# Kernel optimization log

Measured on AMD Instinct MI355X. Metric: run time of the kernel, lower is better.

The kernel has to match this reference:

```python
import jax, jax.numpy as jnp
import numpy as np

B, G, N, D = 8, 16, 256, 768
E, S, SEQ = 1536, 128, 512
EPS = 1e-05


def rope_gn(x):
    # x: [b, g, n, h, s]; positions run over flattened (g, n), matching rope(x, dim=[1,2])
    g, n, half = x.shape[1], x.shape[2], x.shape[-1] // 2
    position = jnp.arange(g * n, dtype=jnp.float32).reshape(g, n)[:, :, None]  # [g,n,1]
    inv_freq = 10000.0 ** (jnp.arange(half, dtype=jnp.float32) / half)
    sinusoid = position[..., None] * inv_freq  # [g,n,1,half]
    sin, cos = jnp.sin(sinusoid), jnp.cos(sinusoid)
    x1, x2 = jnp.split(x, 2, axis=-1)
    return jnp.concatenate([x1 * cos - x2 * sin, x2 * cos + x1 * sin], axis=-1)


def rel_pos_bias(w, seq_len):
    # Toeplitz construction (seq_len <= 512 branch). w: [2*seq_len-1] -> [1, seq_len, seq_len]
    t = jnp.pad(w, (0, seq_len))                  # [3*seq_len-1]
    t = jnp.tile(t, seq_len)[:-seq_len]           # [seq_len*(3*seq_len-2)]
    t = t.reshape(seq_len, 3 * seq_len - 2)
    r = seq_len - 1                                # (2*seq_len-1)//2
    return t[:, r:-r][None]                        # [1, seq_len, seq_len]


def setup_inputs():
    key = jax.random.key(0)
    ks = jax.random.split(key, 8)
    inputs = jax.random.normal(ks[0], (B, G, N, D), dtype=jnp.float32)
    seg = jax.random.randint(ks[1], (B, G * N), 0, 4)
    segment_ids = jnp.sort(seg, axis=-1).reshape(B, G, N)
    params = {
        'ln_w': jnp.ones((D,), jnp.float32),
        'ln_b': jnp.zeros((D,), jnp.float32),
        'W1': jax.random.normal(ks[2], (D, 2 * E + S), jnp.float32) * 0.02,
        'b1': jnp.zeros((2 * E + S,), jnp.float32),
        'gamma': jax.random.uniform(ks[3], (4, S), jnp.float32),
        'beta': jax.random.uniform(ks[4], (4, S), jnp.float32),
        'W2': jax.random.normal(ks[5], (E, D), jnp.float32) * 0.02,
        'b2': jnp.zeros((D,), jnp.float32),
        'w_rel': jax.random.uniform(ks[6], (2 * SEQ - 1,), jnp.float32),
    }
    return dict(inputs=inputs, segment_ids=segment_ids, **params)


def reference(inputs, segment_ids, ln_w, ln_b, W1, b1, gamma, beta, W2, b2, w_rel):
    b, g, n, d = inputs.shape
    shortcut = inputs
    # LayerNorm
    mu = inputs.mean(-1, keepdims=True)
    var = ((inputs - mu) ** 2).mean(-1, keepdims=True)
    x = (inputs - mu) * jax.lax.rsqrt(var + EPS) * ln_w + ln_b
    # dense1 + silu, split into u, v, z
    uv = jax.nn.silu(x @ W1 + b1)
    u, v, z = uv[..., :E], uv[..., E:2 * E], uv[..., 2 * E:]
    # per-head affine gating + rope
    z = z[..., None, :] * gamma + beta            # [b,g,n,4,s]
    z = rope_gn(z)
    quad_q, quad_k, lin_q, lin_k = (z[..., i, :] for i in range(4))
    # non-causal global linear attention
    kv = jnp.einsum('bgcs,bgce->bse', lin_k, v)
    lin_v = jnp.einsum('bgcs,bse->bgce', lin_q, kv)
    lin_kv = jnp.einsum('bgnk,bgne->bgke', lin_k, lin_v) / n
    # segment mask over chunks
    mn = segment_ids.min(-1)
    mx = segment_ids.max(-1)
    mask = ((mn[:, :, None] <= mx[:, None, :]) & (mx[:, :, None] >= mn[:, None, :])).astype(inputs.dtype)
    mask = mask / mask.sum(-1, keepdims=True)
    lin_kv = jnp.einsum('bhke,bgh->bgke', lin_kv, mask)
    linear = jnp.einsum('bgnk,bgke->bgne', lin_q, lin_kv)
    # quadratic relu^2 attention with relative position bias
    qk = jnp.einsum('bgnk,bgmk->bgnm', quad_q, quad_k)
    bias = rel_pos_bias(w_rel, SEQ)[:, :n, :n]    # [1,n,n] broadcasts to [b,g,n,n]
    kernel = jnp.square(jax.nn.relu(qk / n + bias))
    quadratic = jnp.einsum('bgnm,bgme->bgne', kernel, v)
    out = (u * (quadratic + linear)) @ W2 + b2 + shortcut
    return out
```

## Files before the change

### kernel.cpp

```cpp
#include <hip/hip_runtime.h>
#include <math.h>

typedef __bf16 bf16;
typedef __bf16 bf16x8 __attribute__((ext_vector_type(8)));
typedef __bf16 bf16x4 __attribute__((ext_vector_type(4)));
typedef float  f32x4  __attribute__((ext_vector_type(4)));

#define D_   768
#define E_   1536
#define S_   128
#define TT_  32768
#define B_   8

#define OFF_W1T   0UL
#define OFF_W2T   4915200UL
#define OFF_TAB   7274496UL
#define OFF_XN    9375744UL
#define OFF_KER   OFF_XN
#define OFF_QQ    (OFF_XN + 16777216UL)
#define OFF_QK    (OFF_XN + 25165824UL)
#define OFF_LQ    (OFF_XN + 33554432UL)
#define OFF_U     59707392UL
#define OFF_Z     160370688UL
#define OFF_LK    168759296UL
#define OFF_LQT   177147904UL
#define OFF_LKT   185536512UL
#define OFF_MASK  193925120UL
#define OFF_INVF  193933312UL

__device__ __forceinline__ void gl_lds16(const bf16* g, bf16* l) {
  __builtin_amdgcn_global_load_lds(
      (const __attribute__((address_space(1))) unsigned int*)g,
      (__attribute__((address_space(3))) unsigned int*)l, 16, 0, 0);
}


#define STG2(GB, LD, KT, DSTH) do {                                       \
  const int cg_ = (lane & 7) ^ ((lane >> 3) & 7);                         \
  const int rg_ = wave * 32 + ((lane >> 3) << 1) + (cg_ >> 2);            \
  gl_lds16((GB) + (long)rg_ * (LD) + (KT) * 32 + (cg_ & 3) * 8,           \
           (DSTH) + wave * 1024);                                         \
  gl_lds16((GB) + (long)(rg_ + 16) * (LD) + (KT) * 32 + (cg_ & 3) * 8,    \
           (DSTH) + wave * 1024 + 512);                                   \
} while (0)

template <class Epi, bool DUAL, bool SWZ>
__global__ __launch_bounds__(256, 3) void gemm3s(
    const bf16* __restrict__ A, const bf16* __restrict__ B,
    int lda, int ldb, int K,
    long sAb, long sAg, long sBb, long sBg,
    const bf16* __restrict__ A2, const bf16* __restrict__ B2,
    int lda2, int ldb2, int K2,
    long sA2b, long sA2g, long sB2b, long sB2g,
    int gdiv, Epi epi)
{
  __shared__ bf16 smem[3][2][4096];

  const int z = blockIdx.z;
  const int bb = z / gdiv, gg = z % gdiv;

  int bx = blockIdx.x, by = blockIdx.y;
  if constexpr (SWZ) {
    const int nbx = gridDim.x, nby = gridDim.y, nwg = nbx * nby;
    int bid = by * nbx + bx;
    const int q = nwg >> 3, r = nwg & 7;
    const int xcd = bid & 7, lid = bid >> 3;
    bid = (xcd < r ? xcd * (q + 1) : r * (q + 1) + (xcd - r) * q) + lid;
    const int gm = 8;
    const int pig = gm * nby;
    const int grp = bid / pig;
    const int fm = grp * gm;
    const int szm = min(nbx - fm, gm);
    const int loc = bid - grp * pig;
    bx = fm + loc % szm;
    by = loc / szm;
  }

  const int tid  = threadIdx.x;
  const int lane = tid & 63, wave = tid >> 6;
  const int wr = wave >> 1, wc = wave & 1;
  const int lrow = lane & 15, quad = lane >> 4;
  const int lbase = (lrow >> 1) * 128 +
                    (((((lrow & 1) << 2) | quad) ^ ((lrow >> 1) & 7)) * 16);

  f32x4 acc[4][4] = {};
  bf16x8 af[4], bf_[4];

  auto run = [&](const bf16* __restrict__ gA, const bf16* __restrict__ gB,
                 int lda_, int ldb_, int K_, bool first) {
    const int NT = K_ >> 5;
    if (!first) __syncthreads();
    STG2(gA, lda_, 0, &smem[0][0][0]);
    STG2(gB, ldb_, 0, &smem[0][1][0]);
    STG2(gA, lda_, 1, &smem[1][0][0]);
    STG2(gB, ldb_, 1, &smem[1][1][0]);
    asm volatile("s_waitcnt vmcnt(4)" ::: "memory");
    __builtin_amdgcn_s_barrier();
    __builtin_amdgcn_sched_barrier(0);

    int st = 0, sp = 2;
    for (int t = 0; t < NT; ++t) {
      const bf16* aBuf = &smem[st][0][0];
      const bf16* bBuf = &smem[st][1][0];

#pragma unroll
      for (int mi = 0; mi < 4; ++mi)
        af[mi] = *(const bf16x8*)((const char*)aBuf + (wr * 4 + mi) * 1024 + lbase);
#pragma unroll
      for (int ni = 0; ni < 4; ++ni)
        bf_[ni] = *(const bf16x8*)((const char*)bBuf + (wc * 4 + ni) * 1024 + lbase);
      if (t + 2 < NT) {
        STG2(gA, lda_, t + 2, &smem[sp][0][0]);
        STG2(gB, ldb_, t + 2, &smem[sp][1][0]);
      }

      __builtin_amdgcn_s_setprio(1);
#pragma unroll
      for (int mi = 0; mi < 4; ++mi)
#pragma unroll
        for (int ni = 0; ni < 4; ++ni)
          acc[mi][ni] = __builtin_amdgcn_mfma_f32_16x16x32_bf16(
              af[mi], bf_[ni], acc[mi][ni], 0, 0, 0);
      __builtin_amdgcn_s_setprio(0);

      __builtin_amdgcn_sched_barrier(0);
      if (t + 2 < NT)      asm volatile("s_waitcnt vmcnt(4)" ::: "memory");
      else if (t + 1 < NT) asm volatile("s_waitcnt vmcnt(0)" ::: "memory");
      if (t + 1 < NT) {
        __builtin_amdgcn_s_barrier();
        __builtin_amdgcn_sched_barrier(0);
      }
      st = (st == 2) ? 0 : st + 1;
      sp = (sp == 2) ? 0 : sp + 1;
    }
  };

  run(A + bb * sAb + gg * sAg + (long)bx * 128 * lda,
      B + bb * sBb + gg * sBg + (long)by * 128 * ldb, lda, ldb, K, true);
  if constexpr (DUAL)
    run(A2 + bb * sA2b + gg * sA2g + (long)bx * 128 * lda2,
        B2 + bb * sB2b + gg * sB2g + (long)by * 128 * ldb2, lda2, ldb2, K2, false);

  const int rowbase = bx * 128 + wr * 64 + quad * 4;
  const int colbase = by * 128 + wc * 64 + lrow;
#pragma unroll
  for (int mi = 0; mi < 4; mi++)
#pragma unroll
    for (int ni = 0; ni < 4; ni++)
      epi(rowbase + mi * 16, colbase + ni * 16, bb, gg, acc[mi][ni]);
}

struct EpiGemm1 {
  const float* b1; bf16* u; bf16* vT; bf16* z;
  __device__ void operator()(int row0, int col, int, int, f32x4 a) const {
    float s[4];
    const float bias = b1[col];
#pragma unroll
    for (int j = 0; j < 4; j++) {
      float x = a[j] + bias;
      float e = __expf(-x);
      s[j] = __fdividef(x, 1.f + e);
    }
    if (col < E_) {
#pragma unroll
      for (int j = 0; j < 4; j++) u[(long)(row0 + j) * E_ + col] = (bf16)s[j];
    } else if (col < 2 * E_) {
      const int e = col - E_, b = row0 >> 12, t = row0 & 4095;
      bf16x4 o;
#pragma unroll
      for (int j = 0; j < 4; j++) o[j] = (bf16)s[j];
      *(bf16x4*)&vT[((long)(b * E_ + e)) * 4096 + t] = o;
    } else {
      const int sc = col - 2 * E_;
#pragma unroll
      for (int j = 0; j < 4; j++) z[(long)(row0 + j) * S_ + sc] = (bf16)s[j];
    }
  }
};
struct EpiF32 {
  float* C; long sCb, sCg; int ldc;
  __device__ void operator()(int row0, int col, int bb, int gg, f32x4 a) const {
#pragma unroll
    for (int j = 0; j < 4; j++)
      C[(long)bb * sCb + (long)gg * sCg + (long)(row0 + j) * ldc + col] = a[j];
  }
};
struct EpiBf16 {
  bf16* C; long sCb, sCg; int ldc;
  __device__ void operator()(int row0, int col, int bb, int gg, f32x4 a) const {
#pragma unroll
    for (int j = 0; j < 4; j++)
      C[(long)bb * sCb + (long)gg * sCg + (long)(row0 + j) * ldc + col] = (bf16)a[j];
  }
};
struct EpiKer {
  bf16* C; const float* wrel;
  __device__ void operator()(int row0, int col, int bb, int, f32x4 a) const {
#pragma unroll
    for (int j = 0; j < 4; j++) {
      float v = a[j] * (1.f / 256.f) + wrel[511 + col - (row0 + j)];
      v = fmaxf(v, 0.f);
      C[(long)bb * 65536 + (long)(row0 + j) * 256 + col] = (bf16)(v * v);
    }
  }
};
struct EpiCombine {
  bf16* u;
  __device__ void operator()(int row0, int col, int bb, int gg, f32x4 a) const {
#pragma unroll
    for (int j = 0; j < 4; j++) {
      long idx = ((long)((bb * 16 + gg) * 256 + row0 + j)) * E_ + col;
      u[idx] = (bf16)((float)u[idx] * a[j]);
    }
  }
};
struct EpiFinal {
  float* out; const float* b2; const float* x0;
  __device__ void operator()(int row0, int col, int, int, f32x4 a) const {
#pragma unroll
    for (int j = 0; j < 4; j++) {
      long idx = (long)(row0 + j) * D_ + col;
      out[idx] = a[j] + b2[col] + x0[idx];
    }
  }
};

__global__ __launch_bounds__(256) void kvsum_kernel(
    const bf16* __restrict__ kv4, bf16* __restrict__ kvT)
{
  const long i = (long)blockIdx.x * 256 + threadIdx.x;
  const int s = (int)(i & 127);
  const long esb = i >> 7;
  const bf16* p = kv4 + (esb << 9) + s;
  float v = (float)p[0] + (float)p[128] + (float)p[256] + (float)p[384];
  kvT[i] = (bf16)v;
}

__global__ __launch_bounds__(256) void ln_kernel(
    const float* __restrict__ x, const float* __restrict__ w,
    const float* __restrict__ b, bf16* __restrict__ xn)
{
  const long t = blockIdx.x;
  const float* row = x + t * D_;
  const int tid = threadIdx.x;
  float v0 = row[tid], v1 = row[tid + 256], v2 = row[tid + 512];
  float s = v0 + v1 + v2;
  float sq = v0 * v0 + v1 * v1 + v2 * v2;
#pragma unroll
  for (int off = 32; off; off >>= 1) {
    s  += __shfl_down(s, off, 64);
    sq += __shfl_down(sq, off, 64);
  }
  __shared__ float red[2][4];
  const int wave = tid >> 6, lane = tid & 63;
  if (lane == 0) { red[0][wave] = s; red[1][wave] = sq; }
  __syncthreads();
  s  = red[0][0] + red[0][1] + red[0][2] + red[0][3];
  sq = red[1][0] + red[1][1] + red[1][2] + red[1][3];
  const float mean = s * (1.f / 768.f);
  const float var  = sq * (1.f / 768.f) - mean * mean;
  const float rs   = rsqrtf(var + 1e-5f);
  xn[t * D_ + tid]       = (bf16)((v0 - mean) * rs * w[tid] + b[tid]);
  xn[t * D_ + tid + 256] = (bf16)((v1 - mean) * rs * w[tid + 256] + b[tid + 256]);
  xn[t * D_ + tid + 512] = (bf16)((v2 - mean) * rs * w[tid + 512] + b[tid + 512]);
}

template <class TI>
__global__ __launch_bounds__(256) void transpose_cast(
    const TI* __restrict__ in, bf16* __restrict__ out,
    int R, int C, long sInB, long sOutB)
{
  __shared__ float tile[64][65];
  const TI* ib = in  + (long)blockIdx.z * sInB;
  bf16*     ob = out + (long)blockIdx.z * sOutB;
  const int c0 = blockIdx.x * 64, r0 = blockIdx.y * 64;
  const int lc = threadIdx.x & 63, lr0 = threadIdx.x >> 6;
#pragma unroll
  for (int i = 0; i < 16; i++) {
    int r = lr0 + i * 4;
    tile[r][lc] = (float)ib[(long)(r0 + r) * C + c0 + lc];
  }
  __syncthreads();
#pragma unroll
  for (int i = 0; i < 16; i++) {
    int r = lr0 + i * 4;
    ob[(long)(c0 + r) * R + r0 + lc] = (bf16)tile[lc][r];
  }
}

__global__ __launch_bounds__(256) void rope_table_kernel(
    const float* __restrict__ invf, float2* __restrict__ tab)
{
  int idx = blockIdx.x * 256 + threadIdx.x;
  int p = idx >> 6, i = idx & 63;
  float arg = (float)p * invf[i];
  double a = (double)arg;
  tab[idx] = make_float2((float)sin(a), (float)cos(a));
}

__global__ __launch_bounds__(128) void rope_kernel(
    const bf16* __restrict__ zbuf, const float* __restrict__ gamma,
    const float* __restrict__ beta, const float2* __restrict__ tab,
    bf16* __restrict__ qq, bf16* __restrict__ qk,
    bf16* __restrict__ lq, bf16* __restrict__ lk)
{
  const long t = blockIdx.x;
  const int s = threadIdx.x;
  const int p = (int)(t & 4095);
  const int i = s & 63;
  const float2 sc = tab[p * 64 + i];
  const bf16* zr = zbuf + t * S_;
  const float zlo = (float)zr[i], zhi = (float)zr[i + 64];
  bf16* outs[4] = {qq, qk, lq, lk};
#pragma unroll
  for (int r = 0; r < 4; r++) {
    float zl = zlo * gamma[r * 128 + i]      + beta[r * 128 + i];
    float zh = zhi * gamma[r * 128 + i + 64] + beta[r * 128 + i + 64];
    float val = (s < 64) ? (zl * sc.y - zh * sc.x) : (zh * sc.y + zl * sc.x);
    outs[r][t * S_ + s] = (bf16)val;
  }
}

__global__ __launch_bounds__(64) void mask_kernel(const int* __restrict__ seg, float* __restrict__ mask) {
  __shared__ int mn[16], mx[16];
  const int b = blockIdx.x, tid = threadIdx.x;
  if (tid < 16) {
    const int* p = seg + (long)b * 4096 + tid * 256;
    int lo = p[0], hi = p[0];
    for (int i = 1; i < 256; i++) { int v = p[i]; lo = min(lo, v); hi = max(hi, v); }
    mn[tid] = lo; mx[tid] = hi;
  }
  __syncthreads();
  if (tid < 16) {
    const int g = tid;
    float row[16]; float s = 0.f;
    for (int h = 0; h < 16; h++) {
      float o = (mn[g] <= mx[h] && mx[g] >= mn[h]) ? 1.f : 0.f;
      row[h] = o; s += o;
    }
    const float inv = 1.f / s;
    for (int h = 0; h < 16; h++) mask[((long)b * 16 + g) * 16 + h] = row[h] * inv;
  }
}

__global__ __launch_bounds__(256) void mix_kernel(
    const float* __restrict__ P2, const float* __restrict__ mask, bf16* __restrict__ amix)
{
  const int z = blockIdx.x;
  const int b = z >> 4;
  float m[16];
#pragma unroll
  for (int h = 0; h < 16; h++) m[h] = mask[(long)z * 16 + h] * (1.f / 256.f);
  const float* Pb = P2 + (long)b * 16 * 16384;
  bf16* Ab = amix + (long)z * 16384;
#pragma unroll 4
  for (int j = 0; j < 16; j++) {
    int c = j * 256 + threadIdx.x;
    float ax = 0, ay = 0, az = 0, aw = 0;
#pragma unroll
    for (int h = 0; h < 16; h++) {
      float4 p = ((const float4*)(Pb + (long)h * 16384))[c];
      ax += m[h] * p.x; ay += m[h] * p.y; az += m[h] * p.z; aw += m[h] * p.w;
    }
    bf16x4 o; o[0] = (bf16)ax; o[1] = (bf16)ay; o[2] = (bf16)az; o[3] = (bf16)aw;
    *(bf16x4*)&Ab[(long)c * 4] = o;
  }
}

extern "C" void kernel_launch(void* const* d_in, const int* in_sizes, int n_in,
                              void* d_out, int out_size, void* d_ws, size_t ws_size,
                              hipStream_t stream)
{
  const float* x0    = (const float*)d_in[0];
  const int*   seg   = (const int*)d_in[1];
  const float* lnw   = (const float*)d_in[2];
  const float* lnb   = (const float*)d_in[3];
  const float* W1    = (const float*)d_in[4];
  const float* b1    = (const float*)d_in[5];
  const float* gamma = (const float*)d_in[6];
  const float* beta  = (const float*)d_in[7];
  const float* W2    = (const float*)d_in[8];
  const float* b2    = (const float*)d_in[9];
  const float* wrel  = (const float*)d_in[10];
  float* out = (float*)d_out;
  char* ws = (char*)d_ws;

  bf16*   w1t   = (bf16*)(ws + OFF_W1T);
  bf16*   w2t   = (bf16*)(ws + OFF_W2T);
  float2* tab   = (float2*)(ws + OFF_TAB);
  bf16*   xn    = (bf16*)(ws + OFF_XN);
  bf16*   ker   = (bf16*)(ws + OFF_KER);
  bf16*   qq    = (bf16*)(ws + OFF_QQ);
  bf16*   qk    = (bf16*)(ws + OFF_QK);
  bf16*   kv4   = (bf16*)(ws + OFF_QQ);
  bf16*   lq    = (bf16*)(ws + OFF_LQ);
  bf16*   u     = (bf16*)(ws + OFF_U);
  bf16*   zb    = (bf16*)(ws + OFF_Z);
  float*  P2    = (float*)(ws + OFF_Z);
  bf16*   lk    = (bf16*)(ws + OFF_LK);
  bf16*   T1    = (bf16*)(ws + OFF_LK);
  bf16*   lqT   = (bf16*)(ws + OFF_LQT);
  bf16*   amix  = (bf16*)(ws + OFF_LQT);
  bf16*   kvT   = (bf16*)(ws + OFF_LQT + 4194304UL);
  bf16*   lkT   = (bf16*)(ws + OFF_LKT);
  float*  maskb = (float*)(ws + OFF_MASK);
  float*  invfd = (float*)(ws + OFF_INVF);
  bf16*   vTd   = (bf16*)d_out;

  static float h_invf[64];
  for (int i = 0; i < 64; i++) h_invf[i] = powf(10000.0f, (float)i * (1.0f / 64.0f));
  hipMemcpyAsync(invfd, h_invf, 64 * sizeof(float), hipMemcpyHostToDevice, stream);

  transpose_cast<float><<<dim3(50, 12, 1), 256, 0, stream>>>(W1, w1t, 768, 3200, 0, 0);
  transpose_cast<float><<<dim3(12, 24, 1), 256, 0, stream>>>(W2, w2t, 1536, 768, 0, 0);
  rope_table_kernel<<<1024, 256, 0, stream>>>(invfd, tab);
  mask_kernel<<<8, 64, 0, stream>>>(seg, maskb);

  ln_kernel<<<TT_, 256, 0, stream>>>(x0, lnw, lnb, xn);

  gemm3s<EpiGemm1, false, true><<<dim3(256, 25, 1), 256, 0, stream>>>(
      xn, w1t, 768, 768, 768, 0, 0, 0, 0,
      nullptr, nullptr, 0, 0, 0, 0, 0, 0, 0, 1, EpiGemm1{b1, u, vTd, zb});

  rope_kernel<<<TT_, 128, 0, stream>>>(zb, gamma, beta, tab, qq, qk, lq, lk);

  transpose_cast<bf16><<<dim3(2, 64, 8), 256, 0, stream>>>(lq, lqT, 4096, 128, 524288, 524288);
  transpose_cast<bf16><<<dim3(2, 64, 8), 256, 0, stream>>>(lk, lkT, 4096, 128, 524288, 524288);

  gemm3s<EpiF32, false, false><<<dim3(1, 1, 128), 256, 0, stream>>>(
      lqT, lkT, 4096, 4096, 256, 524288, 256, 524288, 256,
      nullptr, nullptr, 0, 0, 0, 0, 0, 0, 0, 16, EpiF32{P2, 262144, 16384, 128});

  mix_kernel<<<128, 256, 0, stream>>>(P2, maskb, amix);

  gemm3s<EpiKer, false, false><<<dim3(2, 2, 128), 256, 0, stream>>>(
      qq, qk, 128, 128, 128, 32768, 0, 32768, 0,
      nullptr, nullptr, 0, 0, 0, 0, 0, 0, 0, 1, EpiKer{ker, wrel});

  gemm3s<EpiBf16, false, false><<<dim3(12, 1, 32), 256, 0, stream>>>(
      vTd, lkT, 4096, 4096, 1024, 6291456, 1024, 524288, 1024,
      nullptr, nullptr, 0, 0, 0, 0, 0, 0, 0, 4, EpiBf16{kv4, 786432, 128, 512});
  kvsum_kernel<<<6144, 256, 0, stream>>>(kv4, kvT);

  gemm3s<EpiBf16, false, false><<<dim3(2, 1, 128), 256, 0, stream>>>(
      lq, amix, 128, 128, 128, 32768, 0, 16384, 0,
      nullptr, nullptr, 0, 0, 0, 0, 0, 0, 0, 1, EpiBf16{T1, 32768, 0, 128});

  gemm3s<EpiCombine, true, false><<<dim3(2, 12, 128), 256, 0, stream>>>(
      ker, vTd, 256, 4096, 256, 1048576, 65536, 6291456, 256,
      T1, kvT, 128, 128, 128, 524288, 32768, 196608, 0, 16, EpiCombine{u});

  gemm3s<EpiFinal, false, true><<<dim3(256, 6, 1), 256, 0, stream>>>(
      u, w2t, 1536, 1536, 1536, 0, 0, 0, 0,
      nullptr, nullptr, 0, 0, 0, 0, 0, 0, 0, 1, EpiFinal{out, b2, x0});
}
```

Measured before the change: 858.5 us.

## Add 256x128 tile GEMM kernel for the two large projection GEMMs

Introduces a specialized gemm256 kernel where each block computes a 256x128 output tile (each wave handles 128x64 with 8x4 MFMA accumulators) using a 3-stage LDS pipeline holding two A tiles and one B tile. The W1 and W2 projection GEMMs now use it with half as many blocks along M. The larger tile raises arithmetic intensity and reuse of B tiles, and cuts global traffic per FLOP. In exchange it doubles accumulator registers, uses more LDS, and lowers occupancy (launch bounds 2 instead of 3). Fewer, larger blocks may also leave some CUs underused in the final wave.

```diff
diff --git a/kernel.cpp b/kernel.cpp
--- a/kernel.cpp
+++ b/kernel.cpp
@@ -34,7 +34,6 @@
       (__attribute__((address_space(3))) unsigned int*)l, 16, 0, 0);
 }
 
-
 #define STG2(GB, LD, KT, DSTH) do {                                       \
   const int cg_ = (lane & 7) ^ ((lane >> 3) & 7);                         \
   const int rg_ = wave * 32 + ((lane >> 3) << 1) + (cg_ >> 2);            \
@@ -44,20 +43,12 @@
            (DSTH) + wave * 1024 + 512);                                   \
 } while (0)
 
-template <class Epi, bool DUAL, bool SWZ>
-__global__ __launch_bounds__(256, 3) void gemm3s(
+template <class Epi, bool SWZ>
+__global__ __launch_bounds__(256, 2) void gemm256(
     const bf16* __restrict__ A, const bf16* __restrict__ B,
-    int lda, int ldb, int K,
-    long sAb, long sAg, long sBb, long sBg,
-    const bf16* __restrict__ A2, const bf16* __restrict__ B2,
-    int lda2, int ldb2, int K2,
-    long sA2b, long sA2g, long sB2b, long sB2g,
-    int gdiv, Epi epi)
-{
-  __shared__ bf16 smem[3][2][4096];
-
-  const int z = blockIdx.z;
-  const int bb = z / gdiv, gg = z % gdiv;
+    int lda, int ldb, int K, Epi epi)
+{
+  __shared__ bf16 smem[3][3][4096];
 
   int bx = blockIdx.x, by = blockIdx.y;
   if constexpr (SWZ) {
@@ -83,6 +74,105 @@
   const int lbase = (lrow >> 1) * 128 +
                     (((((lrow & 1) << 2) | quad) ^ ((lrow >> 1) & 7)) * 16);
 
+  const bf16* gA0 = A + (long)(bx * 256)       * lda;
+  const bf16* gA1 = A + (long)(bx * 256 + 128) * lda;
+  const bf16* gB  = B + (long)(by * 128)       * ldb;
+
+  f32x4 acc[8][4] = {};
+  bf16x8 af[8], bf_[4];
+
+  const int NT = K >> 5;
+
+  STG2(gA0, lda, 0, &smem[0][0][0]);
+  STG2(gA1, lda, 0, &smem[0][1][0]);
+  STG2(gB,  ldb, 0, &smem[0][2][0]);
+  STG2(gA0, lda, 1, &smem[1][0][0]);
+  STG2(gA1, lda, 1, &smem[1][1][0]);
+  STG2(gB,  ldb, 1, &smem[1][2][0]);
+  asm volatile("s_waitcnt vmcnt(6)" ::: "memory");
+  __builtin_amdgcn_s_barrier();
+  __builtin_amdgcn_sched_barrier(0);
+
+  int st = 0, sp = 2;
+  for (int t = 0; t < NT; ++t) {
+    const bf16* aBuf = &smem[st][wr][0];
+    const bf16* bBuf = &smem[st][2][0];
+
+#pragma unroll
+    for (int mi = 0; mi < 8; ++mi)
+      af[mi] = *(const bf16x8*)((const char*)aBuf + mi * 1024 + lbase);
+#pragma unroll
+    for (int ni = 0; ni < 4; ++ni)
+      bf_[ni] = *(const bf16x8*)((const char*)bBuf + (wc * 4 + ni) * 1024 + lbase);
+    if (t + 2 < NT) {
+      STG2(gA0, lda, t + 2, &smem[sp][0][0]);
+      STG2(gA1, lda, t + 2, &smem[sp][1][0]);
+      STG2(gB,  ldb, t + 2, &smem[sp][2][0]);
+    }
+
+#pragma unroll
+    for (int mi = 0; mi < 8; ++mi)
+#pragma unroll
+      for (int ni = 0; ni < 4; ++ni)
+        acc[mi][ni] = __builtin_amdgcn_mfma_f32_16x16x32_bf16(
+            af[mi], bf_[ni], acc[mi][ni], 0, 0, 0);
+
+    __builtin_amdgcn_sched_barrier(0);
+    if (t + 2 < NT)      asm volatile("s_waitcnt vmcnt(6)" ::: "memory");
+    else if (t + 1 < NT) asm volatile("s_waitcnt vmcnt(0)" ::: "memory");
+    if (t + 1 < NT) __builtin_amdgcn_s_barrier();
+    st = (st == 2) ? 0 : st + 1;
+    sp = (sp == 2) ? 0 : sp + 1;
+  }
+
+  const int rowbase = bx * 256 + wr * 128 + quad * 4;
+  const int colbase = by * 128 + wc * 64 + lrow;
+#pragma unroll
+  for (int mi = 0; mi < 8; mi++)
+#pragma unroll
+    for (int ni = 0; ni < 4; ni++)
+      epi(rowbase + mi * 16, colbase + ni * 16, 0, 0, acc[mi][ni]);
+}
+
+template <class Epi, bool DUAL, bool SWZ>
+__global__ __launch_bounds__(256, 3) void gemm3s(
+    const bf16* __restrict__ A, const bf16* __restrict__ B,
+    int lda, int ldb, int K,
+    long sAb, long sAg, long sBb, long sBg,
+    const bf16* __restrict__ A2, const bf16* __restrict__ B2,
+    int lda2, int ldb2, int K2,
+    long sA2b, long sA2g, long sB2b, long sB2g,
+    int gdiv, Epi epi)
+{
+  __shared__ bf16 smem[3][2][4096];
+
+  const int z = blockIdx.z;
+  const int bb = z / gdiv, gg = z % gdiv;
+
+  int bx = blockIdx.x, by = blockIdx.y;
+  if constexpr (SWZ) {
+    const int nbx = gridDim.x, nby = gridDim.y, nwg = nbx * nby;
+    int bid = by * nbx + bx;
+    const int q = nwg >> 3, r = nwg & 7;
+    const int xcd = bid & 7, lid = bid >> 3;
+    bid = (xcd < r ? xcd * (q + 1) : r * (q + 1) + (xcd - r) * q) + lid;
+    const int gm = 8;
+    const int pig = gm * nby;
+    const int grp = bid / pig;
+    const int fm = grp * gm;
+    const int szm = min(nbx - fm, gm);
+    const int loc = bid - grp * pig;
+    bx = fm + loc % szm;
+    by = loc / szm;
+  }
+
+  const int tid  = threadIdx.x;
+  const int lane = tid & 63, wave = tid >> 6;
+  const int wr = wave >> 1, wc = wave & 1;
+  const int lrow = lane & 15, quad = lane >> 4;
+  const int lbase = (lrow >> 1) * 128 +
+                    (((((lrow & 1) << 2) | quad) ^ ((lrow >> 1) & 7)) * 16);
+
   f32x4 acc[4][4] = {};
   bf16x8 af[4], bf_[4];
 
@@ -102,7 +192,6 @@
     for (int t = 0; t < NT; ++t) {
       const bf16* aBuf = &smem[st][0][0];
       const bf16* bBuf = &smem[st][1][0];
-
 #pragma unroll
       for (int mi = 0; mi < 4; ++mi)
         af[mi] = *(const bf16x8*)((const char*)aBuf + (wr * 4 + mi) * 1024 + lbase);
@@ -418,9 +507,8 @@
 
   ln_kernel<<<TT_, 256, 0, stream>>>(x0, lnw, lnb, xn);
 
-  gemm3s<EpiGemm1, false, true><<<dim3(256, 25, 1), 256, 0, stream>>>(
-      xn, w1t, 768, 768, 768, 0, 0, 0, 0,
-      nullptr, nullptr, 0, 0, 0, 0, 0, 0, 0, 1, EpiGemm1{b1, u, vTd, zb});
+  gemm256<EpiGemm1, true><<<dim3(128, 25), 256, 0, stream>>>(
+      xn, w1t, 768, 768, 768, EpiGemm1{b1, u, vTd, zb});
 
   rope_kernel<<<TT_, 128, 0, stream>>>(zb, gamma, beta, tab, qq, qk, lq, lk);
 
@@ -450,7 +538,6 @@
       ker, vTd, 256, 4096, 256, 1048576, 65536, 6291456, 256,
       T1, kvT, 128, 128, 128, 524288, 32768, 196608, 0, 16, EpiCombine{u});
 
-  gemm3s<EpiFinal, false, true><<<dim3(256, 6, 1), 256, 0, stream>>>(
-      u, w2t, 1536, 1536, 1536, 0, 0, 0, 0,
-      nullptr, nullptr, 0, 0, 0, 0, 0, 0, 0, 1, EpiFinal{out, b2, x0});
-}
+  gemm256<EpiFinal, true><<<dim3(128, 6), 256, 0, stream>>>(
+      u, w2t, 1536, 1536, 1536, EpiFinal{out, b2, x0});
+}
```

Result: slower. 900.6 us (+4.9%).
